# Optimization experiments

Measured on AMD Instinct MI355X. Metric: run time of the kernel, lower is better.

## Reference

```python
import jax, jax.numpy as jnp
import numpy as np

N_NODES = 50000
N_EDGES = 625000
HIDDEN = 128
N_TYPES = 4


def setup_inputs() -> dict:
    key = jax.random.key(0)
    ks = jax.random.split(key, 10)
    s = 1.0 / np.sqrt(HIDDEN)
    return {
        "node_states": jax.random.normal(ks[0], (N_NODES, HIDDEN), dtype=jnp.float32),
        "edge_index": jax.random.randint(ks[1], (2, N_EDGES), 0, N_NODES, dtype=jnp.int64),
        "edge_type": jax.random.randint(ks[2], (N_EDGES,), 0, N_TYPES, dtype=jnp.int64),
        # per-edge-type Linear(hidden, hidden): weight [T, d, d] (torch: y = x @ W.T + b)
        "edge_W": jax.random.uniform(ks[3], (N_TYPES, HIDDEN, HIDDEN), jnp.float32, -s, s),
        "edge_b": jax.random.uniform(ks[4], (N_TYPES, HIDDEN), jnp.float32, -s, s),
        # GRUCell params (torch layout: [3d, d] for r|z|n gates)
        "w_ih": jax.random.uniform(ks[5], (3 * HIDDEN, HIDDEN), jnp.float32, -s, s),
        "w_hh": jax.random.uniform(ks[6], (3 * HIDDEN, HIDDEN), jnp.float32, -s, s),
        "b_ih": jax.random.uniform(ks[7], (3 * HIDDEN,), jnp.float32, -s, s),
        "b_hh": jax.random.uniform(ks[8], (3 * HIDDEN,), jnp.float32, -s, s),
    }


def reference(node_states, edge_index, edge_type, edge_W, edge_b, w_ih, w_hh, b_ih, b_hh):
    num_nodes = node_states.shape[0]
    src, dst = edge_index[0], edge_index[1]
    x_src = node_states[src]  # [E, d] gather of source states

    # per-edge-type linear; small fixed loop over edge types, masked accumulate
    msgs = jnp.zeros_like(x_src)
    for t in range(edge_W.shape[0]):
        m_t = x_src @ edge_W[t].T + edge_b[t]  # [E, d]
        msgs = msgs + jnp.where((edge_type == t)[:, None], m_t, 0.0)

    # scatter-sum messages into destination nodes
    agg = jax.ops.segment_sum(msgs, dst, num_segments=num_nodes)  # [N, d]

    # GRUCell(agg, node_states) — torch semantics
    gi = agg @ w_ih.T + b_ih          # [N, 3d]
    gh = node_states @ w_hh.T + b_hh  # [N, 3d]
    i_r, i_z, i_n = jnp.split(gi, 3, axis=1)
    h_r, h_z, h_n = jnp.split(gh, 3, axis=1)
    r = jax.nn.sigmoid(i_r + h_r)
    z = jax.nn.sigmoid(i_z + h_z)
    n = jnp.tanh(i_n + r * h_n)
    return (1.0 - z) * n + z * node_states
```

## Files before the change

kernel.cpp:

```cpp
#include <hip/hip_runtime.h>


typedef __attribute__((ext_vector_type(8))) short short8;
typedef __attribute__((ext_vector_type(4))) float floatx4;

#define HID 128
#define NTY 4

__device__ __forceinline__ unsigned short f2bf(float f) {
    unsigned int u = __float_as_uint(f);
    unsigned int r = (u + 0x7fffu + ((u >> 16) & 1u)) >> 16;
    return (unsigned short)r;
}
__device__ __forceinline__ float bf2f(unsigned int lo16) {
    return __uint_as_float(lo16 << 16);
}
__device__ __forceinline__ float frcp(float x) { return __builtin_amdgcn_rcpf(x); }


__global__ void prep_kernel(const float* __restrict__ h, unsigned short* __restrict__ hbf,
                            const float* __restrict__ W, unsigned short* __restrict__ Wc,
                            const float* __restrict__ w_ih, const float* __restrict__ w_hh,
                            unsigned short* __restrict__ Wg, float* __restrict__ bias4,
                            const float* __restrict__ b_ih, const float* __restrict__ b_hh,
                            int* __restrict__ deg4, int total4, int nb_cvt, int N4) {
    int b = blockIdx.x, tt = threadIdx.x;
    if (b < nb_cvt) {
        int i = b * 256 + tt;
        if (i < total4) {
            float4 v = ((const float4*)h)[i];
            uint2 o;
            o.x = (unsigned int)f2bf(v.x) | ((unsigned int)f2bf(v.y) << 16);
            o.y = (unsigned int)f2bf(v.z) | ((unsigned int)f2bf(v.w) << 16);
            ((uint2*)hbf)[i] = o;
        }
    } else if (b < nb_cvt + 256) {
        int idx = (b - nb_cvt) * 256 + tt;
        int j = idx >> 9, rem = idx & 511;
        int t = rem >> 7, k = rem & 127;
        Wc[idx] = f2bf(W[(t * HID + j) * HID + k]);
    } else if (b < nb_cvt + 768) {
        int idx = (b - nb_cvt - 256) * 256 + tt;
        int row = idx >> 8, k = idx & 255;
        int j = row >> 2, g = row & 3;
        float v = 0.0f;
        if (g == 0) v = (k < 128) ? w_ih[j * 128 + k]         : w_hh[j * 128 + (k - 128)];
        else if (g == 1) v = (k < 128) ? w_ih[(128 + j) * 128 + k] : w_hh[(128 + j) * 128 + (k - 128)];
        else if (g == 2) v = (k < 128) ? w_ih[(256 + j) * 128 + k] : 0.0f;
        else             v = (k < 128) ? 0.0f : w_hh[(256 + j) * 128 + (k - 128)];
        Wg[idx] = f2bf(v);
    } else if (b == nb_cvt + 768) {
        if (tt < 128) {
            float4 v;
            v.x = b_ih[tt] + b_hh[tt];
            v.y = b_ih[128 + tt] + b_hh[128 + tt];
            v.z = b_ih[256 + tt];
            v.w = b_hh[256 + tt];
            ((float4*)bias4)[tt] = v;
        }
    } else {
        int i = (b - nb_cvt - 769) * 256 + tt;
        if (i < N4) deg4[i] = 0;
    }
}


__global__ void hist4_kernel(const int* __restrict__ dst, const int* __restrict__ ety,
                             int* __restrict__ deg4, int E) {
    int e = blockIdx.x * blockDim.x + threadIdx.x;
    if (e < E) atomicAdd(&deg4[dst[e] * 4 + ety[e]], 1);
}

__global__ void scan_blocks4_kernel(const int* __restrict__ deg, int* __restrict__ rowptr,
                                    int* __restrict__ blocksum, int N4) {
    __shared__ int s[256];
    int t = threadIdx.x;
    int base = blockIdx.x * 1024 + t * 4;
    int v0 = 0, v1 = 0, v2 = 0, v3 = 0;
    if (base + 3 < N4) {
        v0 = deg[base]; v1 = deg[base + 1]; v2 = deg[base + 2]; v3 = deg[base + 3];
    } else {
        if (base < N4) v0 = deg[base];
        if (base + 1 < N4) v1 = deg[base + 1];
        if (base + 2 < N4) v2 = deg[base + 2];
    }
    int sum = v0 + v1 + v2 + v3;
    s[t] = sum;
    __syncthreads();
#pragma unroll
    for (int off = 1; off < 256; off <<= 1) {
        int x = (t >= off) ? s[t - off] : 0;
        __syncthreads();
        s[t] += x;
        __syncthreads();
    }
    int ex = s[t] - sum;
    if (base < N4) rowptr[base] = ex;
    if (base + 1 < N4) rowptr[base + 1] = ex + v0;
    if (base + 2 < N4) rowptr[base + 2] = ex + v0 + v1;
    if (base + 3 < N4) rowptr[base + 3] = ex + v0 + v1 + v2;
    if (t == 255) blocksum[blockIdx.x] = s[255];
}

__global__ void scan_top_kernel(const int* __restrict__ blocksum, int* __restrict__ blockoff, int nb) {
    __shared__ int s[256];
    int t = threadIdx.x;
    int v = (t < nb) ? blocksum[t] : 0;
    s[t] = v;
    __syncthreads();
#pragma unroll
    for (int off = 1; off < 256; off <<= 1) {
        int x = (t >= off) ? s[t - off] : 0;
        __syncthreads();
        s[t] += x;
        __syncthreads();
    }
    if (t < nb) blockoff[t] = s[t] - v;
}

__global__ void finalize4_kernel(int* __restrict__ rowptr, const int* __restrict__ blockoff,
                                 int* __restrict__ cursor, int N4, int E) {
    int i = blockIdx.x * blockDim.x + threadIdx.x;
    if (i >= N4) return;
    int r = rowptr[i] + blockoff[i >> 10];
    rowptr[i] = r;
    cursor[i] = r;
    if (i == 0) rowptr[N4] = E;
}

__global__ void fill4_kernel(const int* __restrict__ src, const int* __restrict__ dst,
                             const int* __restrict__ ety, int* __restrict__ cursor,
                             int* __restrict__ csr, int E) {
    int e = blockIdx.x * blockDim.x + threadIdx.x;
    if (e >= E) return;
    int pos = atomicAdd(&cursor[dst[e] * 4 + ety[e]], 1);
    csr[pos] = src[e];
}


__global__ void gather_s_kernel(const int* __restrict__ rowptr4, const int* __restrict__ csr,
                                const unsigned int* __restrict__ hbu,
                                float4* __restrict__ cnt4, unsigned int* __restrict__ Su, int N) {
    int w = blockIdx.x * (blockDim.x >> 6) + (threadIdx.x >> 6);
    if (w >= N) return;
    int lane = threadIdx.x & 63;
    int b0 = rowptr4[w * 4];
    int b1 = rowptr4[w * 4 + 1];
    int b2 = rowptr4[w * 4 + 2];
    int b3 = rowptr4[w * 4 + 3];
    int b4 = rowptr4[w * 4 + 4];

    float s0 = 0.f, s1 = 0.f;
    float sn0[4], sn1[4];
    int e = b0;
#pragma unroll
    for (int t = 0; t < 4; ++t) {
        int bend = (t == 0) ? b1 : (t == 1) ? b2 : (t == 2) ? b3 : b4;
        for (; e + 8 <= bend; e += 8) {
            int p[8];
            unsigned int u[8];
#pragma unroll
            for (int i = 0; i < 8; ++i) p[i] = csr[e + i];
#pragma unroll
            for (int i = 0; i < 8; ++i) u[i] = hbu[(size_t)p[i] * 64 + lane];
#pragma unroll
            for (int i = 0; i < 8; ++i) {
                s0 += bf2f(u[i] & 0xffffu);
                s1 += bf2f(u[i] >> 16);
            }
        }
        for (; e + 4 <= bend; e += 4) {
            int p[4];
            unsigned int u[4];
#pragma unroll
            for (int i = 0; i < 4; ++i) p[i] = csr[e + i];
#pragma unroll
            for (int i = 0; i < 4; ++i) u[i] = hbu[(size_t)p[i] * 64 + lane];
#pragma unroll
            for (int i = 0; i < 4; ++i) {
                s0 += bf2f(u[i] & 0xffffu);
                s1 += bf2f(u[i] >> 16);
            }
        }
        for (; e < bend; ++e) {
            unsigned int u = hbu[(size_t)csr[e] * 64 + lane];
            s0 += bf2f(u & 0xffffu);
            s1 += bf2f(u >> 16);
        }
        sn0[t] = s0;
        sn1[t] = s1;
    }
    float p0 = 0.f, p1 = 0.f;
    size_t base = (size_t)w * 256 + lane;
#pragma unroll
    for (int t = 0; t < 4; ++t) {
        float a0 = sn0[t] - p0, a1 = sn1[t] - p1;
        p0 = sn0[t]; p1 = sn1[t];
        Su[base + t * 64] = (unsigned int)f2bf(a0) | ((unsigned int)f2bf(a1) << 16);
    }
    if (lane == 0)
        cnt4[w] = make_float4((float)(b1 - b0), (float)(b2 - b1),
                              (float)(b3 - b2), (float)(b4 - b3));
}


__global__ __launch_bounds__(512, 4) void agg_gru(const unsigned short* __restrict__ S,
                                                  const unsigned short* __restrict__ Wc,
                                                  const unsigned short* __restrict__ Wg,
                                                  const unsigned short* __restrict__ hbf,
                                                  const float4* __restrict__ cnt4,
                                                  const float* __restrict__ eb,
                                                  const float4* __restrict__ bias4,
                                                  float* __restrict__ out, int M) {
    __shared__ __align__(16) unsigned char smem[51200];
    unsigned short (*Ss)[136] = (unsigned short (*)[136])smem;
    unsigned short (*Xs)[264] = (unsigned short (*)[264])(smem + 17408);
    float (*Outs)[132] = (float (*)[132])smem;

    const int tid = threadIdx.x;
    const int m0 = blockIdx.x * 64;
    const int lane = tid & 63, w = tid >> 6;
    const int lm = lane & 15, quad = lane >> 4;

#pragma unroll
    for (int p = 0; p < 2; ++p) {
        int li = p * 512 + tid;
        int row = li >> 4, col8 = (li & 15) * 8;
        int gm = m0 + row;
        uint4 v = {0u, 0u, 0u, 0u};
        if (gm < M) v = *(const uint4*)(hbf + (size_t)gm * HID + col8);
        *(uint4*)&Xs[row][128 + col8] = v;
    }

    floatx4 accA[4];
#pragma unroll
    for (int a = 0; a < 4; ++a) accA[a] = (floatx4){0.f, 0.f, 0.f, 0.f};

    for (int c = 0; c < 4; ++c) {
#pragma unroll
        for (int p = 0; p < 2; ++p) {
            int li = p * 512 + tid;
            int row = li >> 4, col8 = (li & 15) * 8;
            int gm = m0 + row;
            uint4 v = {0u, 0u, 0u, 0u};
            if (gm < M) v = *(const uint4*)(S + (size_t)gm * 512 + c * 128 + col8);
            *(uint4*)&Ss[row][col8] = v;
        }
        __syncthreads();
#pragma unroll
        for (int s = 0; s < 4; ++s) {
            short8 bw = *(const short8*)(Wc + (size_t)(w * 16 + lm) * 512 + c * 128 + s * 32 + quad * 8);
#pragma unroll
            for (int mi = 0; mi < 4; ++mi) {
                short8 av = *(const short8*)&Ss[mi * 16 + lm][s * 32 + quad * 8];
                accA[mi] = __builtin_amdgcn_mfma_f32_16x16x32_bf16(av, bw, accA[mi], 0, 0, 0);
            }
        }
        __syncthreads();
    }

    {
        int j = w * 16 + lm;
        float e0 = eb[j], e1 = eb[HID + j], e2 = eb[2 * HID + j], e3 = eb[3 * HID + j];
#pragma unroll
        for (int mi = 0; mi < 4; ++mi) {
#pragma unroll
            for (int r = 0; r < 4; ++r) {
                int nl = mi * 16 + quad * 4 + r;
                int gn = m0 + nl;
                float4 c4 = (gn < M) ? cnt4[gn] : make_float4(0.f, 0.f, 0.f, 0.f);
                float v = accA[mi][r] + c4.x * e0 + c4.y * e1 + c4.z * e2 + c4.w * e3;
                Xs[nl][j] = f2bf(v);
            }
        }
    }
    __syncthreads();

    floatx4 accB[4][4];
#pragma unroll
    for (int a = 0; a < 4; ++a)
#pragma unroll
        for (int b = 0; b < 4; ++b) accB[a][b] = (floatx4){0.f, 0.f, 0.f, 0.f};

#pragma unroll
    for (int ss = 0; ss < 8; ++ss) {
        short8 bfr[4];
#pragma unroll
        for (int ni = 0; ni < 4; ++ni)
            bfr[ni] = *(const short8*)&Xs[ni * 16 + lm][ss * 32 + quad * 8];
        short8 af[4];
#pragma unroll
        for (int mi = 0; mi < 4; ++mi)
            af[mi] = *(const short8*)(Wg + (size_t)(w * 64 + mi * 16 + lm) * 256 + ss * 32 + quad * 8);
#pragma unroll
        for (int mi = 0; mi < 4; ++mi)
#pragma unroll
            for (int ni = 0; ni < 4; ++ni)
                accB[mi][ni] = __builtin_amdgcn_mfma_f32_16x16x32_bf16(af[mi], bfr[ni], accB[mi][ni], 0, 0, 0);
    }

#pragma unroll
    for (int mi = 0; mi < 4; ++mi) {
        int j = w * 16 + mi * 4 + quad;
        float4 bb = bias4[j];
#pragma unroll
        for (int ni = 0; ni < 4; ++ni) {
            int nl = ni * 16 + lm;
            float g0 = accB[mi][ni][0], g1 = accB[mi][ni][1];
            float g2 = accB[mi][ni][2], g3 = accB[mi][ni][3];
            float rr = frcp(1.f + __expf(-(g0 + bb.x)));
            float zz = frcp(1.f + __expf(-(g1 + bb.y)));
            float aa = g2 + bb.z + rr * (g3 + bb.w);
            float nn = 1.f - 2.f * frcp(1.f + __expf(2.f * aa));
            float hv = bf2f((unsigned int)Xs[nl][128 + j]);
            accB[mi][ni][0] = nn + zz * (hv - nn);
        }
    }
    __syncthreads();

#pragma unroll
    for (int mi = 0; mi < 4; ++mi) {
        int j = w * 16 + mi * 4 + quad;
#pragma unroll
        for (int ni = 0; ni < 4; ++ni)
            Outs[ni * 16 + lm][j] = accB[mi][ni][0];
    }
    __syncthreads();

    {
        int row = tid >> 3;
        int c0 = (tid & 7) * 16;
        int node = m0 + row;
        if (node < M) {
            float* dstp = out + (size_t)node * HID + c0;
#pragma unroll
            for (int i = 0; i < 4; ++i)
                *(float4*)(dstp + i * 4) = *(const float4*)&Outs[row][c0 + i * 4];
        }
    }
}


extern "C" void kernel_launch(void* const* d_in, const int* in_sizes, int n_in,
                              void* d_out, int out_size, void* d_ws, size_t ws_size,
                              hipStream_t stream) {
    const float* node_states = (const float*)d_in[0];
    const int*   edge_index  = (const int*)d_in[1];
    const int*   edge_type   = (const int*)d_in[2];
    const float* edge_W      = (const float*)d_in[3];
    const float* edge_b      = (const float*)d_in[4];
    const float* w_ih        = (const float*)d_in[5];
    const float* w_hh        = (const float*)d_in[6];
    const float* b_ih        = (const float*)d_in[7];
    const float* b_hh        = (const float*)d_in[8];

    const int M = in_sizes[0] / HID;
    const int E = in_sizes[1] / 2;
    const int N4 = M * 4;
    const int* src = edge_index;
    const int* dst = edge_index + E;

    char* ws = (char*)d_ws;
    size_t off = 0;
    unsigned short* hbf   = (unsigned short*)(ws + off); off += (size_t)M * HID * 2;
    float*          bias4 = (float*)(ws + off);          off += (size_t)128 * 4 * 4;
    unsigned short* S     = (unsigned short*)(ws + off); off += (size_t)M * 512 * 2;
    unsigned short* Wcat  = (unsigned short*)(ws + off); off += (size_t)128 * 512 * 2;
    unsigned short* Wgru  = (unsigned short*)(ws + off); off += (size_t)512 * 256 * 2;
    float*          cnt4  = (float*)(ws + off);          off += (size_t)M * 4 * 4;
    int* deg4     = (int*)(ws + off); off += (size_t)N4 * 4;
    int* rowptr4  = (int*)(ws + off); off += (size_t)(N4 + 1) * 4;
    int* cursor4  = (int*)(ws + off); off += (size_t)N4 * 4;
    int* blocksum = (int*)(ws + off); off += 256 * 4;
    int* blockoff = (int*)(ws + off); off += 256 * 4;
    int* csr      = (int*)(ws + off); off += (size_t)E * 4;

    const int total4 = M * HID / 4;
    const int nb_cvt = (total4 + 255) / 256;
    const int nb_zero = (N4 + 255) / 256;
    const int nb_scan = (N4 + 1023) / 1024;

    prep_kernel<<<nb_cvt + 769 + nb_zero, 256, 0, stream>>>(
        node_states, hbf, edge_W, Wcat, w_ih, w_hh, Wgru, bias4, b_ih, b_hh,
        deg4, total4, nb_cvt, N4);

    hist4_kernel<<<(E + 255) / 256, 256, 0, stream>>>(dst, edge_type, deg4, E);
    scan_blocks4_kernel<<<nb_scan, 256, 0, stream>>>(deg4, rowptr4, blocksum, N4);
    scan_top_kernel<<<1, 256, 0, stream>>>(blocksum, blockoff, nb_scan);
    finalize4_kernel<<<(N4 + 255) / 256, 256, 0, stream>>>(rowptr4, blockoff, cursor4, N4, E);
    fill4_kernel<<<(E + 255) / 256, 256, 0, stream>>>(src, dst, edge_type, cursor4, csr, E);

    gather_s_kernel<<<(M + 3) / 4, 256, 0, stream>>>(rowptr4, csr, (const unsigned int*)hbf,
                                                     (float4*)cnt4, (unsigned int*)S, M);

    agg_gru<<<(M + 63) / 64, 512, 0, stream>>>(S, Wcat, Wgru, hbf, (const float4*)cnt4,
                                               edge_b, (const float4*)bias4, (float*)d_out, M);
}
```

Measured before the change: 283.3 us.

## Merge per-type gather loops and retile agg_gru to 128-node blocks

The gather kernel now runs one 8-wide unrolled loop across all four edge-type segments instead of separate per-type loops with tail loops. Inside that loop it snapshots the partial sums at the segment boundaries, which cuts tail overhead for short per-type segments. The agg_gru kernel now handles 128 nodes per block. Each wave loads its S rows straight from global memory into registers for the message GEMM, skipping the LDS staging, and the hidden-state operand is read directly from global memory. It also uses XOR-swizzled LDS layouts to avoid bank conflicts. The price is more register pressure, extra per-element boundary compares, and more uncached global reads of the weights.

After: 349.8 us. 23.5% more time.

```diff
diff --git a/kernel.cpp b/kernel.cpp
--- a/kernel.cpp
+++ b/kernel.cpp
@@ -144,58 +144,66 @@
     int w = blockIdx.x * (blockDim.x >> 6) + (threadIdx.x >> 6);
     if (w >= N) return;
     int lane = threadIdx.x & 63;
-    int b0 = rowptr4[w * 4];
-    int b1 = rowptr4[w * 4 + 1];
-    int b2 = rowptr4[w * 4 + 2];
-    int b3 = rowptr4[w * 4 + 3];
-    int b4 = rowptr4[w * 4 + 4];
+    int b0 = __builtin_amdgcn_readfirstlane(rowptr4[w * 4]);
+    int b1 = __builtin_amdgcn_readfirstlane(rowptr4[w * 4 + 1]);
+    int b2 = __builtin_amdgcn_readfirstlane(rowptr4[w * 4 + 2]);
+    int b3 = __builtin_amdgcn_readfirstlane(rowptr4[w * 4 + 3]);
+    int b4 = __builtin_amdgcn_readfirstlane(rowptr4[w * 4 + 4]);
 
     float s0 = 0.f, s1 = 0.f;
-    float sn0[4], sn1[4];
+    float sn0[3], sn1[3];
+
     int e = b0;
-#pragma unroll
-    for (int t = 0; t < 4; ++t) {
-        int bend = (t == 0) ? b1 : (t == 1) ? b2 : (t == 2) ? b3 : b4;
-        for (; e + 8 <= bend; e += 8) {
-            int p[8];
-            unsigned int u[8];
-#pragma unroll
-            for (int i = 0; i < 8; ++i) p[i] = csr[e + i];
-#pragma unroll
-            for (int i = 0; i < 8; ++i) u[i] = hbu[(size_t)p[i] * 64 + lane];
-#pragma unroll
-            for (int i = 0; i < 8; ++i) {
+    while (e + 8 <= b4) {
+        int p[8];
+        unsigned int u[8];
+#pragma unroll
+        for (int i = 0; i < 8; ++i) p[i] = csr[e + i];
+#pragma unroll
+        for (int i = 0; i < 8; ++i) u[i] = hbu[(size_t)p[i] * 64 + lane];
+#pragma unroll
+        for (int i = 0; i < 8; ++i) {
+            int idx = e + i;
+            if (idx == b1) { sn0[0] = s0; sn1[0] = s1; }
+            if (idx == b2) { sn0[1] = s0; sn1[1] = s1; }
+            if (idx == b3) { sn0[2] = s0; sn1[2] = s1; }
+            s0 += bf2f(u[i] & 0xffffu);
+            s1 += bf2f(u[i] >> 16);
+        }
+        e += 8;
+    }
+    {
+        int rem = b4 - e;
+        int p[7];
+        unsigned int u[7];
+#pragma unroll
+        for (int i = 0; i < 7; ++i) if (i < rem) p[i] = csr[e + i];
+#pragma unroll
+        for (int i = 0; i < 7; ++i) if (i < rem) u[i] = hbu[(size_t)p[i] * 64 + lane];
+#pragma unroll
+        for (int i = 0; i < 7; ++i) {
+            if (i < rem) {
+                int idx = e + i;
+                if (idx == b1) { sn0[0] = s0; sn1[0] = s1; }
+                if (idx == b2) { sn0[1] = s0; sn1[1] = s1; }
+                if (idx == b3) { sn0[2] = s0; sn1[2] = s1; }
                 s0 += bf2f(u[i] & 0xffffu);
                 s1 += bf2f(u[i] >> 16);
             }
         }
-        for (; e + 4 <= bend; e += 4) {
-            int p[4];
-            unsigned int u[4];
-#pragma unroll
-            for (int i = 0; i < 4; ++i) p[i] = csr[e + i];
-#pragma unroll
-            for (int i = 0; i < 4; ++i) u[i] = hbu[(size_t)p[i] * 64 + lane];
-#pragma unroll
-            for (int i = 0; i < 4; ++i) {
-                s0 += bf2f(u[i] & 0xffffu);
-                s1 += bf2f(u[i] >> 16);
-            }
-        }
-        for (; e < bend; ++e) {
-            unsigned int u = hbu[(size_t)csr[e] * 64 + lane];
-            s0 += bf2f(u & 0xffffu);
-            s1 += bf2f(u >> 16);
-        }
-        sn0[t] = s0;
-        sn1[t] = s1;
-    }
-    float p0 = 0.f, p1 = 0.f;
+    }
+    if (b1 == b4) { sn0[0] = s0; sn1[0] = s1; }
+    if (b2 == b4) { sn0[1] = s0; sn1[1] = s1; }
+    if (b3 == b4) { sn0[2] = s0; sn1[2] = s1; }
+
     size_t base = (size_t)w * 256 + lane;
+    float a0, a1, p0 = 0.f, p1 = 0.f;
 #pragma unroll
     for (int t = 0; t < 4; ++t) {
-        float a0 = sn0[t] - p0, a1 = sn1[t] - p1;
-        p0 = sn0[t]; p1 = sn1[t];
+        float c0 = (t < 3) ? sn0[t] : s0;
+        float c1 = (t < 3) ? sn1[t] : s1;
+        a0 = c0 - p0; a1 = c1 - p1;
+        p0 = c0; p1 = c1;
         Su[base + t * 64] = (unsigned int)f2bf(a0) | ((unsigned int)f2bf(a1) << 16);
     }
     if (lane == 0)
@@ -212,131 +220,123 @@
                                                   const float* __restrict__ eb,
                                                   const float4* __restrict__ bias4,
                                                   float* __restrict__ out, int M) {
-    __shared__ __align__(16) unsigned char smem[51200];
-    unsigned short (*Ss)[136] = (unsigned short (*)[136])smem;
-    unsigned short (*Xs)[264] = (unsigned short (*)[264])(smem + 17408);
-    float (*Outs)[132] = (float (*)[132])smem;
+    __shared__ __align__(16) unsigned short Xagg[128][128];
+    __shared__ __align__(16) float Outs[64][128];
 
     const int tid = threadIdx.x;
-    const int m0 = blockIdx.x * 64;
+    const int m0 = blockIdx.x * 128;
     const int lane = tid & 63, w = tid >> 6;
     const int lm = lane & 15, quad = lane >> 4;
 
-#pragma unroll
+    floatx4 accA[8];
+#pragma unroll
+    for (int n = 0; n < 8; ++n) accA[n] = (floatx4){0.f, 0.f, 0.f, 0.f};
+
+    int arow = m0 + w * 16 + lm;
+    if (arow >= M) arow = M - 1;
+    const unsigned short* Sp = S + (size_t)arow * 512 + quad * 8;
+
+#pragma unroll
+    for (int ks = 0; ks < 16; ++ks) {
+        short8 av = *(const short8*)(Sp + ks * 32);
+#pragma unroll
+        for (int n = 0; n < 8; ++n) {
+            short8 bw = *(const short8*)(Wc + (size_t)(n * 16 + lm) * 512 + ks * 32 + quad * 8);
+            accA[n] = __builtin_amdgcn_mfma_f32_16x16x32_bf16(av, bw, accA[n], 0, 0, 0);
+        }
+    }
+
+    {
+        float4 c4v[4];
+#pragma unroll
+        for (int r = 0; r < 4; ++r) {
+            int gn = m0 + w * 16 + quad * 4 + r;
+            if (gn >= M) gn = M - 1;
+            c4v[r] = cnt4[gn];
+        }
+#pragma unroll
+        for (int n = 0; n < 8; ++n) {
+            int j = n * 16 + lm;
+            float e0 = eb[j], e1 = eb[HID + j], e2 = eb[2 * HID + j], e3 = eb[3 * HID + j];
+#pragma unroll
+            for (int r = 0; r < 4; ++r) {
+                int nl = w * 16 + quad * 4 + r;
+                float v = accA[n][r] + c4v[r].x * e0 + c4v[r].y * e1 + c4v[r].z * e2 + c4v[r].w * e3;
+                Xagg[nl][j ^ ((nl & 7) << 3)] = f2bf(v);
+            }
+        }
+    }
+    __syncthreads();
+
+#pragma unroll 1
     for (int p = 0; p < 2; ++p) {
-        int li = p * 512 + tid;
-        int row = li >> 4, col8 = (li & 15) * 8;
-        int gm = m0 + row;
-        uint4 v = {0u, 0u, 0u, 0u};
-        if (gm < M) v = *(const uint4*)(hbf + (size_t)gm * HID + col8);
-        *(uint4*)&Xs[row][128 + col8] = v;
-    }
-
-    floatx4 accA[4];
-#pragma unroll
-    for (int a = 0; a < 4; ++a) accA[a] = (floatx4){0.f, 0.f, 0.f, 0.f};
-
-    for (int c = 0; c < 4; ++c) {
-#pragma unroll
-        for (int p = 0; p < 2; ++p) {
-            int li = p * 512 + tid;
-            int row = li >> 4, col8 = (li & 15) * 8;
-            int gm = m0 + row;
-            uint4 v = {0u, 0u, 0u, 0u};
-            if (gm < M) v = *(const uint4*)(S + (size_t)gm * 512 + c * 128 + col8);
-            *(uint4*)&Ss[row][col8] = v;
-        }
-        __syncthreads();
-#pragma unroll
-        for (int s = 0; s < 4; ++s) {
-            short8 bw = *(const short8*)(Wc + (size_t)(w * 16 + lm) * 512 + c * 128 + s * 32 + quad * 8);
-#pragma unroll
-            for (int mi = 0; mi < 4; ++mi) {
-                short8 av = *(const short8*)&Ss[mi * 16 + lm][s * 32 + quad * 8];
-                accA[mi] = __builtin_amdgcn_mfma_f32_16x16x32_bf16(av, bw, accA[mi], 0, 0, 0);
-            }
-        }
-        __syncthreads();
-    }
-
-    {
-        int j = w * 16 + lm;
-        float e0 = eb[j], e1 = eb[HID + j], e2 = eb[2 * HID + j], e3 = eb[3 * HID + j];
+        floatx4 accB[4][4];
+#pragma unroll
+        for (int a = 0; a < 4; ++a)
+#pragma unroll
+            for (int b = 0; b < 4; ++b) accB[a][b] = (floatx4){0.f, 0.f, 0.f, 0.f};
+
+#pragma unroll
+        for (int ss = 0; ss < 8; ++ss) {
+            short8 bfr[4];
+#pragma unroll
+            for (int ni = 0; ni < 4; ++ni) {
+                if (ss < 4) {
+                    int row = p * 64 + ni * 16 + lm;
+                    int col = (ss * 32 + quad * 8) ^ ((lm & 7) << 3);
+                    bfr[ni] = *(const short8*)&Xagg[row][col];
+                } else {
+                    int gr = m0 + p * 64 + ni * 16 + lm;
+                    if (gr >= M) gr = M - 1;
+                    bfr[ni] = *(const short8*)(hbf + (size_t)gr * HID + (ss - 4) * 32 + quad * 8);
+                }
+            }
+            short8 af[4];
+#pragma unroll
+            for (int mi = 0; mi < 4; ++mi)
+                af[mi] = *(const short8*)(Wg + (size_t)(w * 64 + mi * 16 + lm) * 256 + ss * 32 + quad * 8);
+#pragma unroll
+            for (int mi = 0; mi < 4; ++mi)
+#pragma unroll
+                for (int ni = 0; ni < 4; ++ni)
+                    accB[mi][ni] = __builtin_amdgcn_mfma_f32_16x16x32_bf16(af[mi], bfr[ni], accB[mi][ni], 0, 0, 0);
+        }
+
 #pragma unroll
         for (int mi = 0; mi < 4; ++mi) {
-#pragma unroll
-            for (int r = 0; r < 4; ++r) {
-                int nl = mi * 16 + quad * 4 + r;
-                int gn = m0 + nl;
-                float4 c4 = (gn < M) ? cnt4[gn] : make_float4(0.f, 0.f, 0.f, 0.f);
-                float v = accA[mi][r] + c4.x * e0 + c4.y * e1 + c4.z * e2 + c4.w * e3;
-                Xs[nl][j] = f2bf(v);
-            }
-        }
-    }
-    __syncthreads();
-
-    floatx4 accB[4][4];
-#pragma unroll
-    for (int a = 0; a < 4; ++a)
-#pragma unroll
-        for (int b = 0; b < 4; ++b) accB[a][b] = (floatx4){0.f, 0.f, 0.f, 0.f};
-
-#pragma unroll
-    for (int ss = 0; ss < 8; ++ss) {
-        short8 bfr[4];
-#pragma unroll
-        for (int ni = 0; ni < 4; ++ni)
-            bfr[ni] = *(const short8*)&Xs[ni * 16 + lm][ss * 32 + quad * 8];
-        short8 af[4];
-#pragma unroll
-        for (int mi = 0; mi < 4; ++mi)
-            af[mi] = *(const short8*)(Wg + (size_t)(w * 64 + mi * 16 + lm) * 256 + ss * 32 + quad * 8);
-#pragma unroll
-        for (int mi = 0; mi < 4; ++mi)
-#pragma unroll
-            for (int ni = 0; ni < 4; ++ni)
-                accB[mi][ni] = __builtin_amdgcn_mfma_f32_16x16x32_bf16(af[mi], bfr[ni], accB[mi][ni], 0, 0, 0);
-    }
-
-#pragma unroll
-    for (int mi = 0; mi < 4; ++mi) {
-        int j = w * 16 + mi * 4 + quad;
-        float4 bb = bias4[j];
-#pragma unroll
-        for (int ni = 0; ni < 4; ++ni) {
-            int nl = ni * 16 + lm;
-            float g0 = accB[mi][ni][0], g1 = accB[mi][ni][1];
-            float g2 = accB[mi][ni][2], g3 = accB[mi][ni][3];
-            float rr = frcp(1.f + __expf(-(g0 + bb.x)));
-            float zz = frcp(1.f + __expf(-(g1 + bb.y)));
-            float aa = g2 + bb.z + rr * (g3 + bb.w);
-            float nn = 1.f - 2.f * frcp(1.f + __expf(2.f * aa));
-            float hv = bf2f((unsigned int)Xs[nl][128 + j]);
-            accB[mi][ni][0] = nn + zz * (hv - nn);
-        }
-    }
-    __syncthreads();
-
-#pragma unroll
-    for (int mi = 0; mi < 4; ++mi) {
-        int j = w * 16 + mi * 4 + quad;
-#pragma unroll
-        for (int ni = 0; ni < 4; ++ni)
-            Outs[ni * 16 + lm][j] = accB[mi][ni][0];
-    }
-    __syncthreads();
-
-    {
-        int row = tid >> 3;
-        int c0 = (tid & 7) * 16;
-        int node = m0 + row;
-        if (node < M) {
-            float* dstp = out + (size_t)node * HID + c0;
-#pragma unroll
-            for (int i = 0; i < 4; ++i)
-                *(float4*)(dstp + i * 4) = *(const float4*)&Outs[row][c0 + i * 4];
-        }
+            int j = w * 16 + mi * 4 + quad;
+            float4 bb = bias4[j];
+#pragma unroll
+            for (int ni = 0; ni < 4; ++ni) {
+                int nl = ni * 16 + lm;
+                int gn = m0 + p * 64 + nl;
+                int gc = (gn >= M) ? (M - 1) : gn;
+                float g0 = accB[mi][ni][0], g1 = accB[mi][ni][1];
+                float g2 = accB[mi][ni][2], g3 = accB[mi][ni][3];
+                float rr = frcp(1.f + __expf(-(g0 + bb.x)));
+                float zz = frcp(1.f + __expf(-(g1 + bb.y)));
+                float aa = g2 + bb.z + rr * (g3 + bb.w);
+                float nn = 1.f - 2.f * frcp(1.f + __expf(2.f * aa));
+                float hv = bf2f((unsigned int)hbf[(size_t)gc * HID + j]);
+                Outs[nl][j ^ ((nl & 7) << 2)] = nn + zz * (hv - nn);
+            }
+        }
+        __syncthreads();
+
+        {
+            int row = tid >> 3;
+            int c0 = (tid & 7) * 16;
+            int node = m0 + p * 64 + row;
+            if (node < M) {
+                float* dstp = out + (size_t)node * HID;
+#pragma unroll
+                for (int i = 0; i < 4; ++i) {
+                    int c = c0 + i * 4;
+                    *(float4*)(dstp + c) = *(const float4*)&Outs[row][c ^ ((row & 7) << 2)];
+                }
+            }
+        }
+        __syncthreads();
     }
 }
 
@@ -393,6 +393,6 @@
     gather_s_kernel<<<(M + 3) / 4, 256, 0, stream>>>(rowptr4, csr, (const unsigned int*)hbf,
                                                      (float4*)cnt4, (unsigned int*)S, M);
 
-    agg_gru<<<(M + 63) / 64, 512, 0, stream>>>(S, Wcat, Wgru, hbf, (const float4*)cnt4,
-                                               edge_b, (const float4*)bias4, (float*)d_out, M);
-}
+    agg_gru<<<(M + 127) / 128, 512, 0, stream>>>(S, Wcat, Wgru, hbf, (const float4*)cnt4,
+                                                 edge_b, (const float4*)bias4, (float*)d_out, M);
+}
```
